# Kernel tuning notes

Hardware: AMD Instinct MI355X
Metric: run time of the kernel (lower is better)

The kernel has to match this reference:

```python
import jax, jax.numpy as jnp
import numpy as np
from jax import lax

T, N, H, A = 128, 64, 1024, 16  # timesteps, batch(envs), hidden_size, num_actions


def _ortho(key, shape):
    # approximate nn.init.orthogonal_ via QR of a gaussian
    a = jax.random.normal(key, shape, dtype=jnp.float32)
    flip = shape[0] < shape[1]
    q, r = jnp.linalg.qr(a.T if flip else a)
    q = q * jnp.sign(jnp.diagonal(r))
    return (q.T if flip else q).astype(jnp.float32)


def setup_inputs() -> dict:
    key = jax.random.key(0)
    ks = jax.random.split(key, 10)
    c = jax.random.normal(ks[0], (T * N, H), dtype=jnp.float32)
    hxs = jax.random.normal(ks[1], (N, 2 * H), dtype=jnp.float32)
    masks = jnp.ones((T * N, 1), dtype=jnp.float32)
    prev_action_one_hot = jax.random.uniform(ks[2], (T * N, A), dtype=jnp.float32)
    # GRUCell params (torch layout: weight_ih [3H, in], weight_hh [3H, H])
    w_ih_h = _ortho(ks[3], (3 * H, H))
    w_hh_h = _ortho(ks[4], (3 * H, H))
    b_ih_h = jnp.zeros((3 * H,), dtype=jnp.float32)
    b_hh_h = jnp.zeros((3 * H,), dtype=jnp.float32)
    w_ih_p = _ortho(ks[5], (3 * H, H))
    w_hh_p = _ortho(ks[6], (3 * H, H))
    b_ih_p = jnp.zeros((3 * H,), dtype=jnp.float32)
    b_hh_p = jnp.zeros((3 * H,), dtype=jnp.float32)
    # p_network: Linear(H+A, H) -> tanh -> Linear(H, A)
    p_w1 = jax.random.normal(ks[7], (H, H + A), dtype=jnp.float32) / np.sqrt(H + A)
    p_b1 = jnp.zeros((H,), dtype=jnp.float32)
    p_w2 = jax.random.normal(ks[8], (A, H), dtype=jnp.float32) / np.sqrt(H)
    p_b2 = jnp.zeros((A,), dtype=jnp.float32)
    return dict(c=c, hxs=hxs, masks=masks, prev_action_one_hot=prev_action_one_hot,
                w_ih_h=w_ih_h, w_hh_h=w_hh_h, b_ih_h=b_ih_h, b_hh_h=b_hh_h,
                w_ih_p=w_ih_p, w_hh_p=w_hh_p, b_ih_p=b_ih_p, b_hh_p=b_hh_p,
                p_w1=p_w1, p_b1=p_b1, p_w2=p_w2, p_b2=p_b2)


def _gru_cell(x, h, w_ih, w_hh, b_ih, b_hh):
    # torch.nn.GRUCell semantics
    gi = x @ w_ih.T + b_ih  # [N, 3H]
    gh = h @ w_hh.T + b_hh  # [N, 3H]
    i_r, i_z, i_n = jnp.split(gi, 3, axis=1)
    h_r, h_z, h_n = jnp.split(gh, 3, axis=1)
    r = jax.nn.sigmoid(i_r + h_r)
    z = jax.nn.sigmoid(i_z + h_z)
    n = jnp.tanh(i_n + r * h_n)
    return (1.0 - z) * n + z * h


def reference(c, hxs, masks, prev_action_one_hot,
              w_ih_h, w_hh_h, b_ih_h, b_hh_h,
              w_ih_p, w_hh_p, b_ih_p, b_hh_p,
              p_w1, p_b1, p_w2, p_b2):
    c3 = c.reshape(T, N, H)
    m3 = masks.reshape(T, N, 1)
    a3 = prev_action_one_hot.reshape(T, N, A)
    h0 = hxs[:, :H]
    pol0 = hxs[:, H:]

    def step(carry, xs):
        h, pol = carry
        c_t, m_t, a_t = xs
        p_in = jnp.concatenate([h, a_t], axis=1) * m_t
        p_dist = jnp.tanh(p_in @ p_w1.T + p_b1) @ p_w2.T + p_b2  # [N, A]
        h = _gru_cell(c_t, h * m_t, w_ih_h, w_hh_h, b_ih_h, b_hh_h)
        pol = _gru_cell(c_t, pol * m_t, w_ih_p, w_hh_p, b_ih_p, b_hh_p)
        return (h, pol), (p_dist, pol)

    (h, pol), (acc_p_dist, acc_policy) = lax.scan(step, (h0, pol0), (c3, m3, a3))
    acc_p_dist = acc_p_dist.reshape(T * N, -1)
    acc_policy = acc_policy.reshape(T * N, -1)
    hxs_out = jnp.concatenate([h, pol], axis=1)
    return acc_p_dist, acc_policy, hxs_out
```

## Files before the change

### kernel.cpp

```cpp
#include <hip/hip_runtime.h>
#include <hip/hip_bf16.h>
#include <math.h>

#define TT 128
#define NN 64
#define HH 1024
#define AA 16
#define G3 3072
#define NC 6144
#define PK 1088
#define WLDS_STRIDE 1032
#define GISL 3072

#define PD_OFF  0
#define POL_OFF (TT*NN*AA)
#define HXS_OFF (POL_OFF + TT*NN*HH)

typedef __attribute__((ext_vector_type(8))) short short8;
typedef __attribute__((ext_vector_type(4))) float f32x4;

__device__ __align__(16) __hip_bfloat16 g_c_bf[TT*NN*HH];
__device__ __align__(16) __hip_bfloat16 g_wihc_bf[NC*HH];
__device__ __align__(16) __hip_bfloat16 g_whh_bf[2][G3*HH];
__device__ __align__(16) __hip_bfloat16 g_pw1_bf[HH*PK];
__device__ __align__(16) __hip_bfloat16 g_pw2_bf[AA*HH];
__device__ float g_gi2[(size_t)2*64*TT*GISL];
__device__ float g_h[NN*HH];
__device__ float g_pol[NN*HH];
__device__ __align__(16) __hip_bfloat16 g_pin_all[(size_t)(TT+1)*NN*PK];
__device__ __align__(16) __hip_bfloat16 g_polm_all[(size_t)(TT+1)*NN*HH];
__device__ __align__(16) __hip_bfloat16 g_ph_all[TT*NN*HH];

__device__ __align__(256) unsigned g_flagsA[2][64];
__device__ __align__(256) unsigned g_gi_cnt[64];

__device__ __forceinline__ float sigmoidf_(float x) { return 1.0f / (1.0f + __expf(-x)); }
__device__ __forceinline__ float tanhf_(float x) {
  float e = __expf(2.0f * x);
  return 1.0f - 2.0f / (e + 1.0f);
}

__global__ __launch_bounds__(256) void conv_all(
    const float* __restrict__ c, const float* __restrict__ masks, const float* __restrict__ act,
    const float* __restrict__ wih_h, const float* __restrict__ wih_p,
    const float* __restrict__ whh_h, const float* __restrict__ whh_p,
    const float* __restrict__ pw1, const float* __restrict__ pw2)
{
  size_t i = (size_t)blockIdx.x * 256 + threadIdx.x;
  size_t stride = (size_t)gridDim.x * 256;
  for (size_t f = i; f < (size_t)TT*NN*HH; f += stride) g_c_bf[f] = __float2bfloat16(c[f]);
  for (size_t f = i; f < (size_t)G3*HH; f += stride) {
    g_wihc_bf[f]                 = __float2bfloat16(wih_h[f]);
    g_wihc_bf[(size_t)G3*HH + f] = __float2bfloat16(wih_p[f]);
    g_whh_bf[0][f] = __float2bfloat16(whh_h[f]);
    g_whh_bf[1][f] = __float2bfloat16(whh_p[f]);
  }
  for (size_t f = i; f < (size_t)HH*PK; f += stride) {
    int o = (int)(f / PK), j = (int)(f % PK);
    g_pw1_bf[f] = (j < HH + AA) ? __float2bfloat16(pw1[(size_t)o*(HH+AA) + j]) : __float2bfloat16(0.0f);
  }
  for (size_t f = i; f < (size_t)AA*HH; f += stride) g_pw2_bf[f] = __float2bfloat16(pw2[f]);
  for (size_t f = i; f < (size_t)TT*NN*(PK-HH); f += stride) {
    int row = (int)(f >> 6), j = (int)(f & 63);
    float v = (j < AA) ? act[(size_t)row*AA + j] * masks[row] : 0.0f;
    g_pin_all[(size_t)row*PK + HH + j] = __float2bfloat16(v);
  }
}

__global__ __launch_bounds__(256) void init_kernel(const float* __restrict__ hxs,
                                                   const float* __restrict__ masks) {
  int f = blockIdx.x * 256 + threadIdx.x;
  int n = f >> 10, j = f & 1023;
  float m0 = masks[n];
  float hv = hxs[n * 2 * HH + j];
  float pv = hxs[n * 2 * HH + HH + j];
  g_h[f] = hv;
  g_pol[f] = pv;
  g_pin_all[(size_t)n * PK + j]  = __float2bfloat16(hv * m0);
  g_polm_all[(size_t)n * HH + j] = __float2bfloat16(pv * m0);
  if (f < 128)
    __hip_atomic_store(&g_flagsA[f >> 6][f & 63], 0u,
                       __ATOMIC_RELAXED, __HIP_MEMORY_SCOPE_AGENT);
  if (f >= 128 && f < 192)
    __hip_atomic_store(&g_gi_cnt[f - 128], 0u,
                       __ATOMIC_RELAXED, __HIP_MEMORY_SCOPE_AGENT);
}

__global__ __launch_bounds__(256, 1) void fused_scan(
    const float* __restrict__ masks,
    const float* __restrict__ bih_h, const float* __restrict__ bhh_h,
    const float* __restrict__ bih_p, const float* __restrict__ bhh_p,
    float* __restrict__ out)
{
  extern __shared__ __align__(16) __hip_bfloat16 Dyn[];
  __shared__ float m_lds[TT * NN];
  __shared__ __align__(8) __hip_bfloat16 sL[NN * 16];
  const int tid = threadIdx.x, l = tid & 63, w = tid >> 6;

  if (blockIdx.x < 128) {
    __hip_bfloat16* Ws = Dyn;
    const int gru = blockIdx.x >> 6;
    const int idx = blockIdx.x & 63;
    const int c0  = idx * 16;
    const __hip_bfloat16* __restrict__ W = g_whh_bf[gru];

    for (int i = tid; i < TT * NN; i += 256) m_lds[i] = masks[i];

    for (int ch = tid; ch < 48 * 128; ch += 256) {
      int row = ch >> 7, ko = (ch & 127) * 8;
      int gate = row >> 4, j = row & 15;
      *(short8*)(&Ws[row * WLDS_STRIDE + ko]) =
          *(const short8*)(W + (size_t)(gate * HH + c0 + j) * HH + ko);
    }
    __syncthreads();

    const float* bi = (gru == 0) ? bih_h : bih_p;
    const float* bh = (gru == 0) ? bhh_h : bhh_p;
    const int col = c0 + (l & 15);
    const float bir = bi[col],        bhr = bh[col];
    const float biz = bi[HH + col],   bhz = bh[HH + col];
    const float bin = bi[2*HH + col], bhn = bh[2*HH + col];
    const int rowbase = w * 16 + (l >> 4) * 4;
    const int arow = w * 16 + (l & 15);
    const int lo8 = (l >> 4) * 8;
    const int jj = l & 15;

    float hst[4];
    {
      const float* st0 = (gru == 0) ? g_h : g_pol;
#pragma unroll
      for (int reg = 0; reg < 4; ++reg) hst[reg] = st0[(rowbase + reg) * HH + col];
    }

    while (__hip_atomic_load(&g_gi_cnt[0], __ATOMIC_RELAXED,
                             __HIP_MEMORY_SCOPE_AGENT) < 48u) { }
    const float* __restrict__ gib = g_gi2 + (size_t)(gru * 64 + idx) * TT * GISL;
    float gir[4], giz[4], gin[4];
#pragma unroll
    for (int reg = 0; reg < 4; ++reg) {
      const float* gp = gib + (size_t)(rowbase + reg) * 48;
      gir[reg] = gp[jj]; giz[reg] = gp[16 + jj]; gin[reg] = gp[32 + jj];
    }

    const int astr = (gru == 0) ? PK : HH;
    volatile unsigned* __restrict__ myflags = g_flagsA[gru];

    for (int t = 0; t < TT; ++t) {
      const __hip_bfloat16* __restrict__ Ab =
          (gru == 0) ? (g_pin_all + (size_t)t * NN * PK)
                     : (g_polm_all + (size_t)t * NN * HH);
      const __hip_bfloat16* __restrict__ arowp = Ab + (size_t)arow * astr + lo8;

      short8 av[32];
#pragma unroll
      for (int u = 0; u < 32; ++u) av[u] = *(const short8*)(arowp + u * 32);

      f32x4 acc0 = {}, acc1 = {}, acc2 = {};
#pragma unroll
      for (int u = 0; u < 32; ++u) {
        short8 b0  = *(const short8*)(&Ws[( 0 + jj) * WLDS_STRIDE + u * 32 + lo8]);
        short8 b1  = *(const short8*)(&Ws[(16 + jj) * WLDS_STRIDE + u * 32 + lo8]);
        short8 bn2 = *(const short8*)(&Ws[(32 + jj) * WLDS_STRIDE + u * 32 + lo8]);
        acc0 = __builtin_amdgcn_mfma_f32_16x16x32_bf16(av[u], b0,  acc0, 0, 0, 0);
        acc1 = __builtin_amdgcn_mfma_f32_16x16x32_bf16(av[u], b1,  acc1, 0, 0, 0);
        acc2 = __builtin_amdgcn_mfma_f32_16x16x32_bf16(av[u], bn2, acc2, 0, 0, 0);
      }

      float hv_out[4];
#pragma unroll
      for (int reg = 0; reg < 4; ++reg) {
        int row = rowbase + reg;
        float mk  = m_lds[t * NN + row];
        float mk1 = (t < TT - 1) ? m_lds[(t + 1) * NN + row] : 1.0f;
        float hm = hst[reg] * mk;
        float rg  = sigmoidf_(gir[reg] + acc0[reg] + bir + bhr);
        float z   = sigmoidf_(giz[reg] + acc1[reg] + biz + bhz);
        float nn2 = tanhf_  (gin[reg] + bin + rg * (acc2[reg] + bhn));
        float hv = (1.0f - z) * nn2 + z * hm;
        hst[reg] = hv;
        hv_out[reg] = hv;
        sL[row * 16 + jj] = __float2bfloat16(hv * mk1);
      }

      __syncthreads();
      {
        int rr = tid >> 2, cc = tid & 3;
        unsigned long long v = *(const unsigned long long*)(&sL[rr * 16 + cc * 4]);
        __hip_bfloat16* dstp = (gru == 0)
            ? (g_pin_all + (size_t)(t + 1) * NN * PK + (size_t)rr * PK + c0 + cc * 4)
            : (g_polm_all + (size_t)(t + 1) * NN * HH + (size_t)rr * HH + c0 + cc * 4);
        __hip_atomic_store((unsigned long long*)dstp, v,
                           __ATOMIC_RELAXED, __HIP_MEMORY_SCOPE_AGENT);
      }

      if (t < TT - 1) {
        asm volatile("s_waitcnt vmcnt(0)" ::: "memory");
        __syncthreads();
        if (tid == 0)
          __hip_atomic_store((unsigned*)&g_flagsA[gru][idx], (unsigned)(t + 1),
                             __ATOMIC_RELAXED, __HIP_MEMORY_SCOPE_AGENT);
        if (gru == 1) {
#pragma unroll
          for (int reg = 0; reg < 4; ++reg)
            out[POL_OFF + (size_t)(t * NN + rowbase + reg) * HH + col] = hv_out[reg];
        }
        {
          const int slab = (t + 1) >> 1;
          while (__hip_atomic_load(&g_gi_cnt[slab], __ATOMIC_RELAXED,
                                   __HIP_MEMORY_SCOPE_AGENT) < 48u) { }
          const float* gpt = gib + (size_t)(t + 1) * GISL;
#pragma unroll
          for (int reg = 0; reg < 4; ++reg) {
            const float* gp = gpt + (size_t)(rowbase + reg) * 48;
            gir[reg] = gp[jj]; giz[reg] = gp[16 + jj]; gin[reg] = gp[32 + jj];
          }
        }
        while (__hip_atomic_load((const unsigned*)&myflags[l], __ATOMIC_RELAXED,
                                 __HIP_MEMORY_SCOPE_AGENT) < (unsigned)(t + 1)) { }
      } else {
        if (gru == 1) {
#pragma unroll
          for (int reg = 0; reg < 4; ++reg)
            out[POL_OFF + (size_t)(t * NN + rowbase + reg) * HH + col] = hv_out[reg];
        }
      }
    }

    float* stf = (gru == 0) ? g_h : g_pol;
#pragma unroll
    for (int reg = 0; reg < 4; ++reg) stf[(rowbase + reg) * HH + col] = hst[reg];

  } else {
    __hip_bfloat16* AsD = Dyn;
    __hip_bfloat16* BsD = Dyn + 2 * 128 * 72;
    const int roff = (w >> 1) * 64, coff = (w & 1) * 64;

    for (int kt2 = 0; kt2 < 24; ++kt2) {
      const int tile = (blockIdx.x - 128) + (kt2 << 7);
      const int bm = tile / 48, bn = tile % 48;
      const __hip_bfloat16* A = g_c_bf    + (size_t)bm * 128 * HH;
      const __hip_bfloat16* B = g_wihc_bf + (size_t)bn * 128 * HH;

      short8 ra[4], rb[4];
#define PG_LOAD(KT) { _Pragma("unroll") for (int q = 0; q < 4; ++q) { \
    int cch = q * 256 + tid; int row = cch >> 3, ko = (cch & 7) * 8; \
    ra[q] = *(const short8*)(A + (size_t)row * HH + (KT) * 64 + ko); \
    rb[q] = *(const short8*)(B + (size_t)row * HH + (KT) * 64 + ko); } }
#define PG_STORE(BUF) { _Pragma("unroll") for (int q = 0; q < 4; ++q) { \
    int cch = q * 256 + tid; int row = cch >> 3, ko = (cch & 7) * 8; \
    *(short8*)(AsD + (BUF) * 9216 + row * 72 + ko) = ra[q]; \
    *(short8*)(BsD + (BUF) * 9216 + row * 72 + ko) = rb[q]; } }

      __syncthreads();
      PG_LOAD(0); PG_STORE(0);
      f32x4 acc[4][4] = {};
      for (int kt = 0; kt < 16; ++kt) {
        __syncthreads();
        if (kt < 15) PG_LOAD(kt + 1);
        const int buf = kt & 1;
#pragma unroll
        for (int ks = 0; ks < 2; ++ks) {
          short8 a[4], b[4];
#pragma unroll
          for (int fr = 0; fr < 4; ++fr)
            a[fr] = *(const short8*)(AsD + buf * 9216 + (roff + fr * 16 + (l & 15)) * 72 + ks * 32 + (l >> 4) * 8);
#pragma unroll
          for (int fc = 0; fc < 4; ++fc)
            b[fc] = *(const short8*)(BsD + buf * 9216 + (coff + fc * 16 + (l & 15)) * 72 + ks * 32 + (l >> 4) * 8);
#pragma unroll
          for (int fr = 0; fr < 4; ++fr)
#pragma unroll
            for (int fc = 0; fc < 4; ++fc)
              acc[fr][fc] = __builtin_amdgcn_mfma_f32_16x16x32_bf16(a[fr], b[fc], acc[fr][fc], 0, 0, 0);
        }
        if (kt < 15) PG_STORE((kt + 1) & 1);
      }
#pragma unroll
      for (int fr = 0; fr < 4; ++fr)
#pragma unroll
        for (int fc = 0; fc < 4; ++fc) {
          int colg = bn * 128 + coff + fc * 16 + (l & 15);
          int q2 = colg >> 10;
          int gru2 = (q2 >= 3), gate = q2 - 3 * gru2;
          int hcol = colg & 1023, cb = hcol >> 4, j = hcol & 15;
#pragma unroll
          for (int reg = 0; reg < 4; ++reg) {
            int grow = bm * 128 + roff + fr * 16 + (l >> 4) * 4 + reg;
            int tt2 = grow >> 6, n = grow & 63;
            __hip_atomic_store(
                &g_gi2[((size_t)(gru2 * 64 + cb) * TT + tt2) * GISL + n * 48 + gate * 16 + j],
                acc[fr][fc][reg], __ATOMIC_RELAXED, __HIP_MEMORY_SCOPE_AGENT);
          }
        }
      asm volatile("s_waitcnt vmcnt(0)" ::: "memory");
      __syncthreads();
      if (tid == 0)
        __hip_atomic_fetch_add(&g_gi_cnt[bm], 1u,
                               __ATOMIC_RELAXED, __HIP_MEMORY_SCOPE_AGENT);
    }
  }
}

__global__ __launch_bounds__(256) void pol_gemm(const float* __restrict__ pb1) {
  __shared__ __align__(16) __hip_bfloat16 As[2][128 * 72];
  __shared__ __align__(16) __hip_bfloat16 Bs[2][128 * 72];
  const int tid = threadIdx.x, l = tid & 63, w = tid >> 6;
  const int bm = blockIdx.x / 8, bn = blockIdx.x % 8;
  const __hip_bfloat16* A = g_pin_all + (size_t)bm * 128 * PK;
  const __hip_bfloat16* B = g_pw1_bf  + (size_t)bn * 128 * PK;
  const int roff = (w >> 1) * 64, coff = (w & 1) * 64;

  short8 ra[4], rb[4];
#define PL_LOAD(KT) { _Pragma("unroll") for (int q = 0; q < 4; ++q) { \
    int cch = q * 256 + tid; int row = cch >> 3, ko = (cch & 7) * 8; \
    ra[q] = *(const short8*)(A + (size_t)row * PK + (KT) * 64 + ko); \
    rb[q] = *(const short8*)(B + (size_t)row * PK + (KT) * 64 + ko); } }
#define PL_STORE(BUF) { _Pragma("unroll") for (int q = 0; q < 4; ++q) { \
    int cch = q * 256 + tid; int row = cch >> 3, ko = (cch & 7) * 8; \
    *(short8*)(&As[BUF][row * 72 + ko]) = ra[q]; \
    *(short8*)(&Bs[BUF][row * 72 + ko]) = rb[q]; } }

  PL_LOAD(0); PL_STORE(0);
  f32x4 acc[4][4] = {};
  for (int kt = 0; kt < 17; ++kt) {
    __syncthreads();
    if (kt < 16) PL_LOAD(kt + 1);
    const int buf = kt & 1;
#pragma unroll
    for (int ks = 0; ks < 2; ++ks) {
      short8 a[4], b[4];
#pragma unroll
      for (int fr = 0; fr < 4; ++fr)
        a[fr] = *(const short8*)(&As[buf][(roff + fr * 16 + (l & 15)) * 72 + ks * 32 + (l >> 4) * 8]);
#pragma unroll
      for (int fc = 0; fc < 4; ++fc)
        b[fc] = *(const short8*)(&Bs[buf][(coff + fc * 16 + (l & 15)) * 72 + ks * 32 + (l >> 4) * 8]);
#pragma unroll
      for (int fr = 0; fr < 4; ++fr)
#pragma unroll
        for (int fc = 0; fc < 4; ++fc)
          acc[fr][fc] = __builtin_amdgcn_mfma_f32_16x16x32_bf16(a[fr], b[fc], acc[fr][fc], 0, 0, 0);
    }
    if (kt < 16) PL_STORE((kt + 1) & 1);
  }
#pragma unroll
  for (int fc = 0; fc < 4; ++fc) {
    int col = bn * 128 + coff + fc * 16 + (l & 15);
    float b1v = pb1[col];
#pragma unroll
    for (int fr = 0; fr < 4; ++fr)
#pragma unroll
      for (int reg = 0; reg < 4; ++reg) {
        int row = bm * 128 + roff + fr * 16 + (l >> 4) * 4 + reg;
        g_ph_all[(size_t)row * HH + col] = __float2bfloat16(tanhf_(acc[fr][fc][reg] + b1v));
      }
  }
}

__global__ __launch_bounds__(256) void pdist_kernel(const float* __restrict__ pb2,
                                                    float* __restrict__ out) {
  const int tid = threadIdx.x, l = tid & 63, w = tid >> 6;
  const int r0 = blockIdx.x * 64;
  f32x4 pa = {};
  const __hip_bfloat16* PH = g_ph_all + (size_t)(r0 + w * 16 + (l & 15)) * HH;
  const __hip_bfloat16* B  = g_pw2_bf + (size_t)(l & 15) * HH;
#pragma unroll 4
  for (int k32 = 0; k32 < 32; ++k32) {
    short8 a = *(const short8*)(PH + k32 * 32 + (l >> 4) * 8);
    short8 b = *(const short8*)(B  + k32 * 32 + (l >> 4) * 8);
    pa = __builtin_amdgcn_mfma_f32_16x16x32_bf16(a, b, pa, 0, 0, 0);
  }
  int o = l & 15;
  float bb = pb2[o];
#pragma unroll
  for (int reg = 0; reg < 4; ++reg) {
    int row = r0 + w * 16 + (l >> 4) * 4 + reg;
    out[PD_OFF + (size_t)row * AA + o] = pa[reg] + bb;
  }
}

__global__ __launch_bounds__(256) void final_kernel(float* __restrict__ out) {
  int f = blockIdx.x * 256 + threadIdx.x;
  int n = f >> 11, j = f & 2047;
  out[HXS_OFF + f] = (j < HH) ? g_h[n * HH + j] : g_pol[n * HH + (j - HH)];
}

extern "C" void kernel_launch(void* const* d_in, const int* in_sizes, int n_in,
                              void* d_out, int out_size, void* d_ws, size_t ws_size,
                              hipStream_t stream) {
  const float* c     = (const float*)d_in[0];
  const float* hxs   = (const float*)d_in[1];
  const float* masks = (const float*)d_in[2];
  const float* act   = (const float*)d_in[3];
  const float* wih_h = (const float*)d_in[4];
  const float* whh_h = (const float*)d_in[5];
  const float* bih_h = (const float*)d_in[6];
  const float* bhh_h = (const float*)d_in[7];
  const float* wih_p = (const float*)d_in[8];
  const float* whh_p = (const float*)d_in[9];
  const float* bih_p = (const float*)d_in[10];
  const float* bhh_p = (const float*)d_in[11];
  const float* pw1   = (const float*)d_in[12];
  const float* pb1   = (const float*)d_in[13];
  const float* pw2   = (const float*)d_in[14];
  const float* pb2   = (const float*)d_in[15];
  float* out = (float*)d_out;

  const int dyn_bytes = 48 * WLDS_STRIDE * 2;
  (void)hipFuncSetAttribute((const void*)fused_scan,
                            hipFuncAttributeMaxDynamicSharedMemorySize, dyn_bytes);

  conv_all<<<4096, 256, 0, stream>>>(c, masks, act, wih_h, wih_p, whh_h, whh_p, pw1, pw2);
  init_kernel<<<256, 256, 0, stream>>>(hxs, masks);
  fused_scan<<<256, 256, dyn_bytes, stream>>>(masks, bih_h, bhh_h, bih_p, bhh_p, out);
  pol_gemm<<<512, 256, 0, stream>>>(pb1);
  pdist_kernel<<<128, 256, 0, stream>>>(pb2, out);
  final_kernel<<<512, 256, 0, stream>>>(out);
}
```

Measured before the change: 1.223 ms.

## Fuse policy GEMM and pdist into scan kernel's idle helper blocks

```diff
diff --git a/kernel.cpp b/kernel.cpp
--- a/kernel.cpp
+++ b/kernel.cpp
@@ -21,7 +21,6 @@
 
 __device__ __align__(16) __hip_bfloat16 g_c_bf[TT*NN*HH];
 __device__ __align__(16) __hip_bfloat16 g_wihc_bf[NC*HH];
-__device__ __align__(16) __hip_bfloat16 g_whh_bf[2][G3*HH];
 __device__ __align__(16) __hip_bfloat16 g_pw1_bf[HH*PK];
 __device__ __align__(16) __hip_bfloat16 g_pw2_bf[AA*HH];
 __device__ float g_gi2[(size_t)2*64*TT*GISL];
@@ -33,6 +32,7 @@
 
 __device__ __align__(256) unsigned g_flagsA[2][64];
 __device__ __align__(256) unsigned g_gi_cnt[64];
+__device__ __align__(256) unsigned g_pol_cnt[64];
 
 __device__ __forceinline__ float sigmoidf_(float x) { return 1.0f / (1.0f + __expf(-x)); }
 __device__ __forceinline__ float tanhf_(float x) {
@@ -43,7 +43,6 @@
 __global__ __launch_bounds__(256) void conv_all(
     const float* __restrict__ c, const float* __restrict__ masks, const float* __restrict__ act,
     const float* __restrict__ wih_h, const float* __restrict__ wih_p,
-    const float* __restrict__ whh_h, const float* __restrict__ whh_p,
     const float* __restrict__ pw1, const float* __restrict__ pw2)
 {
   size_t i = (size_t)blockIdx.x * 256 + threadIdx.x;
@@ -52,8 +51,6 @@
   for (size_t f = i; f < (size_t)G3*HH; f += stride) {
     g_wihc_bf[f]                 = __float2bfloat16(wih_h[f]);
     g_wihc_bf[(size_t)G3*HH + f] = __float2bfloat16(wih_p[f]);
-    g_whh_bf[0][f] = __float2bfloat16(whh_h[f]);
-    g_whh_bf[1][f] = __float2bfloat16(whh_p[f]);
   }
   for (size_t f = i; f < (size_t)HH*PK; f += stride) {
     int o = (int)(f / PK), j = (int)(f % PK);
@@ -84,12 +81,17 @@
   if (f >= 128 && f < 192)
     __hip_atomic_store(&g_gi_cnt[f - 128], 0u,
                        __ATOMIC_RELAXED, __HIP_MEMORY_SCOPE_AGENT);
+  if (f >= 192 && f < 256)
+    __hip_atomic_store(&g_pol_cnt[f - 192], 0u,
+                       __ATOMIC_RELAXED, __HIP_MEMORY_SCOPE_AGENT);
 }
 
 __global__ __launch_bounds__(256, 1) void fused_scan(
     const float* __restrict__ masks,
+    const float* __restrict__ whh_h, const float* __restrict__ whh_p,
     const float* __restrict__ bih_h, const float* __restrict__ bhh_h,
     const float* __restrict__ bih_p, const float* __restrict__ bhh_p,
+    const float* __restrict__ pb1, const float* __restrict__ pb2,
     float* __restrict__ out)
 {
   extern __shared__ __align__(16) __hip_bfloat16 Dyn[];
@@ -102,15 +104,18 @@
     const int gru = blockIdx.x >> 6;
     const int idx = blockIdx.x & 63;
     const int c0  = idx * 16;
-    const __hip_bfloat16* __restrict__ W = g_whh_bf[gru];
+    const float* __restrict__ Wf = (gru == 0) ? whh_h : whh_p;
 
     for (int i = tid; i < TT * NN; i += 256) m_lds[i] = masks[i];
 
     for (int ch = tid; ch < 48 * 128; ch += 256) {
       int row = ch >> 7, ko = (ch & 127) * 8;
       int gate = row >> 4, j = row & 15;
-      *(short8*)(&Ws[row * WLDS_STRIDE + ko]) =
-          *(const short8*)(W + (size_t)(gate * HH + c0 + j) * HH + ko);
+      const float* s = Wf + (size_t)(gate * HH + c0 + j) * HH + ko;
+      union { short8 v; __hip_bfloat16 hh[8]; } tmp;
+#pragma unroll
+      for (int q = 0; q < 8; ++q) tmp.hh[q] = __float2bfloat16(s[q]);
+      *(short8*)(&Ws[row * WLDS_STRIDE + ko]) = tmp.v;
     }
     __syncthreads();
 
@@ -132,8 +137,11 @@
       for (int reg = 0; reg < 4; ++reg) hst[reg] = st0[(rowbase + reg) * HH + col];
     }
 
+    unsigned gi_ready = 0;
     while (__hip_atomic_load(&g_gi_cnt[0], __ATOMIC_RELAXED,
                              __HIP_MEMORY_SCOPE_AGENT) < 48u) { }
+    asm volatile("" ::: "memory");
+    gi_ready = 1;
     const float* __restrict__ gib = g_gi2 + (size_t)(gru * 64 + idx) * TT * GISL;
     float gir[4], giz[4], gin[4];
 #pragma unroll
@@ -143,7 +151,6 @@
     }
 
     const int astr = (gru == 0) ? PK : HH;
-    volatile unsigned* __restrict__ myflags = g_flagsA[gru];
 
     for (int t = 0; t < TT; ++t) {
       const __hip_bfloat16* __restrict__ Ab =
@@ -151,9 +158,22 @@
                      : (g_polm_all + (size_t)t * NN * HH);
       const __hip_bfloat16* __restrict__ arowp = Ab + (size_t)arow * astr + lo8;
 
+      unsigned fv = __hip_atomic_load(&g_flagsA[gru][l], __ATOMIC_RELAXED,
+                                      __HIP_MEMORY_SCOPE_AGENT);
+      unsigned long long rdy = __ballot(fv >= (unsigned)t);
       short8 av[32];
 #pragma unroll
-      for (int u = 0; u < 32; ++u) av[u] = *(const short8*)(arowp + u * 32);
+      for (int g = 0; g < 8; ++g) {
+        while (((rdy >> (g * 8)) & 0xFFull) != 0xFFull) {
+          fv = __hip_atomic_load(&g_flagsA[gru][l], __ATOMIC_RELAXED,
+                                 __HIP_MEMORY_SCOPE_AGENT);
+          rdy = __ballot(fv >= (unsigned)t);
+        }
+        asm volatile("" ::: "memory");
+#pragma unroll
+        for (int q = 0; q < 4; ++q)
+          av[g * 4 + q] = *(const short8*)(arowp + (g * 4 + q) * 32);
+      }
 
       f32x4 acc0 = {}, acc1 = {}, acc2 = {};
 #pragma unroll
@@ -192,10 +212,10 @@
         __hip_atomic_store((unsigned long long*)dstp, v,
                            __ATOMIC_RELAXED, __HIP_MEMORY_SCOPE_AGENT);
       }
+      asm volatile("s_waitcnt vmcnt(0)" ::: "memory");
+      __syncthreads();
 
       if (t < TT - 1) {
-        asm volatile("s_waitcnt vmcnt(0)" ::: "memory");
-        __syncthreads();
         if (tid == 0)
           __hip_atomic_store((unsigned*)&g_flagsA[gru][idx], (unsigned)(t + 1),
                              __ATOMIC_RELAXED, __HIP_MEMORY_SCOPE_AGENT);
@@ -205,9 +225,13 @@
             out[POL_OFF + (size_t)(t * NN + rowbase + reg) * HH + col] = hv_out[reg];
         }
         {
-          const int slab = (t + 1) >> 1;
-          while (__hip_atomic_load(&g_gi_cnt[slab], __ATOMIC_RELAXED,
-                                   __HIP_MEMORY_SCOPE_AGENT) < 48u) { }
+          const unsigned slab = (unsigned)((t + 1) >> 1);
+          if (slab >= gi_ready) {
+            while (__hip_atomic_load(&g_gi_cnt[slab], __ATOMIC_RELAXED,
+                                     __HIP_MEMORY_SCOPE_AGENT) < 48u) { }
+            asm volatile("" ::: "memory");
+            gi_ready = slab + 1;
+          }
           const float* gpt = gib + (size_t)(t + 1) * GISL;
 #pragma unroll
           for (int reg = 0; reg < 4; ++reg) {
@@ -215,8 +239,6 @@
             gir[reg] = gp[jj]; giz[reg] = gp[16 + jj]; gin[reg] = gp[32 + jj];
           }
         }
-        while (__hip_atomic_load((const unsigned*)&myflags[l], __ATOMIC_RELAXED,
-                                 __HIP_MEMORY_SCOPE_AGENT) < (unsigned)(t + 1)) { }
       } else {
         if (gru == 1) {
 #pragma unroll
@@ -234,46 +256,41 @@
     __hip_bfloat16* AsD = Dyn;
     __hip_bfloat16* BsD = Dyn + 2 * 128 * 72;
     const int roff = (w >> 1) * 64, coff = (w & 1) * 64;
+    const int pid = blockIdx.x - 128;
 
     for (int kt2 = 0; kt2 < 24; ++kt2) {
-      const int tile = (blockIdx.x - 128) + (kt2 << 7);
+      const int tile = pid + (kt2 << 7);
       const int bm = tile / 48, bn = tile % 48;
       const __hip_bfloat16* A = g_c_bf    + (size_t)bm * 128 * HH;
       const __hip_bfloat16* B = g_wihc_bf + (size_t)bn * 128 * HH;
 
       short8 ra[4], rb[4];
-#define PG_LOAD(KT) { _Pragma("unroll") for (int q = 0; q < 4; ++q) { \
+#define PG_LOAD(KT, AP, BP, STR) { _Pragma("unroll") for (int q = 0; q < 4; ++q) { \
     int cch = q * 256 + tid; int row = cch >> 3, ko = (cch & 7) * 8; \
-    ra[q] = *(const short8*)(A + (size_t)row * HH + (KT) * 64 + ko); \
-    rb[q] = *(const short8*)(B + (size_t)row * HH + (KT) * 64 + ko); } }
+    ra[q] = *(const short8*)((AP) + (size_t)row * (STR) + (KT) * 64 + ko); \
+    rb[q] = *(const short8*)((BP) + (size_t)row * (STR) + (KT) * 64 + ko); } }
 #define PG_STORE(BUF) { _Pragma("unroll") for (int q = 0; q < 4; ++q) { \
     int cch = q * 256 + tid; int row = cch >> 3, ko = (cch & 7) * 8; \
     *(short8*)(AsD + (BUF) * 9216 + row * 72 + ko) = ra[q]; \
     *(short8*)(BsD + (BUF) * 9216 + row * 72 + ko) = rb[q]; } }
-
-      __syncthreads();
-      PG_LOAD(0); PG_STORE(0);
+#define PG_MMA(BUF) { _Pragma("unroll") for (int ks = 0; ks < 2; ++ks) { \
+      short8 a[4], b[4]; \
+      _Pragma("unroll") for (int fr = 0; fr < 4; ++fr) \
+        a[fr] = *(const short8*)(AsD + (BUF) * 9216 + (roff + fr * 16 + (l & 15)) * 72 + ks * 32 + (l >> 4) * 8); \
+      _Pragma("unroll") for (int fc = 0; fc < 4; ++fc) \
+        b[fc] = *(const short8*)(BsD + (BUF) * 9216 + (coff + fc * 16 + (l & 15)) * 72 + ks * 32 + (l >> 4) * 8); \
+      _Pragma("unroll") for (int fr = 0; fr < 4; ++fr) \
+        _Pragma("unroll") for (int fc = 0; fc < 4; ++fc) \
+          acc[fr][fc] = __builtin_amdgcn_mfma_f32_16x16x32_bf16(a[fr], b[fc], acc[fr][fc], 0, 0, 0); } }
+
+      __syncthreads();
+      PG_LOAD(0, A, B, HH) PG_STORE(0)
       f32x4 acc[4][4] = {};
       for (int kt = 0; kt < 16; ++kt) {
         __syncthreads();
-        if (kt < 15) PG_LOAD(kt + 1);
-        const int buf = kt & 1;
-#pragma unroll
-        for (int ks = 0; ks < 2; ++ks) {
-          short8 a[4], b[4];
-#pragma unroll
-          for (int fr = 0; fr < 4; ++fr)
-            a[fr] = *(const short8*)(AsD + buf * 9216 + (roff + fr * 16 + (l & 15)) * 72 + ks * 32 + (l >> 4) * 8);
-#pragma unroll
-          for (int fc = 0; fc < 4; ++fc)
-            b[fc] = *(const short8*)(BsD + buf * 9216 + (coff + fc * 16 + (l & 15)) * 72 + ks * 32 + (l >> 4) * 8);
-#pragma unroll
-          for (int fr = 0; fr < 4; ++fr)
-#pragma unroll
-            for (int fc = 0; fc < 4; ++fc)
-              acc[fr][fc] = __builtin_amdgcn_mfma_f32_16x16x32_bf16(a[fr], b[fc], acc[fr][fc], 0, 0, 0);
-        }
-        if (kt < 15) PG_STORE((kt + 1) & 1);
+        if (kt < 15) PG_LOAD(kt + 1, A, B, HH)
+        PG_MMA(kt & 1)
+        if (kt < 15) PG_STORE((kt + 1) & 1)
       }
 #pragma unroll
       for (int fr = 0; fr < 4; ++fr)
@@ -298,84 +315,77 @@
         __hip_atomic_fetch_add(&g_gi_cnt[bm], 1u,
                                __ATOMIC_RELAXED, __HIP_MEMORY_SCOPE_AGENT);
     }
-  }
-}
-
-__global__ __launch_bounds__(256) void pol_gemm(const float* __restrict__ pb1) {
-  __shared__ __align__(16) __hip_bfloat16 As[2][128 * 72];
-  __shared__ __align__(16) __hip_bfloat16 Bs[2][128 * 72];
-  const int tid = threadIdx.x, l = tid & 63, w = tid >> 6;
-  const int bm = blockIdx.x / 8, bn = blockIdx.x % 8;
-  const __hip_bfloat16* A = g_pin_all + (size_t)bm * 128 * PK;
-  const __hip_bfloat16* B = g_pw1_bf  + (size_t)bn * 128 * PK;
-  const int roff = (w >> 1) * 64, coff = (w & 1) * 64;
-
-  short8 ra[4], rb[4];
-#define PL_LOAD(KT) { _Pragma("unroll") for (int q = 0; q < 4; ++q) { \
-    int cch = q * 256 + tid; int row = cch >> 3, ko = (cch & 7) * 8; \
-    ra[q] = *(const short8*)(A + (size_t)row * PK + (KT) * 64 + ko); \
-    rb[q] = *(const short8*)(B + (size_t)row * PK + (KT) * 64 + ko); } }
-#define PL_STORE(BUF) { _Pragma("unroll") for (int q = 0; q < 4; ++q) { \
-    int cch = q * 256 + tid; int row = cch >> 3, ko = (cch & 7) * 8; \
-    *(short8*)(&As[BUF][row * 72 + ko]) = ra[q]; \
-    *(short8*)(&Bs[BUF][row * 72 + ko]) = rb[q]; } }
-
-  PL_LOAD(0); PL_STORE(0);
-  f32x4 acc[4][4] = {};
-  for (int kt = 0; kt < 17; ++kt) {
-    __syncthreads();
-    if (kt < 16) PL_LOAD(kt + 1);
-    const int buf = kt & 1;
-#pragma unroll
-    for (int ks = 0; ks < 2; ++ks) {
-      short8 a[4], b[4];
-#pragma unroll
-      for (int fr = 0; fr < 4; ++fr)
-        a[fr] = *(const short8*)(&As[buf][(roff + fr * 16 + (l & 15)) * 72 + ks * 32 + (l >> 4) * 8]);
-#pragma unroll
-      for (int fc = 0; fc < 4; ++fc)
-        b[fc] = *(const short8*)(&Bs[buf][(coff + fc * 16 + (l & 15)) * 72 + ks * 32 + (l >> 4) * 8]);
-#pragma unroll
-      for (int fr = 0; fr < 4; ++fr)
-#pragma unroll
-        for (int fc = 0; fc < 4; ++fc)
-          acc[fr][fc] = __builtin_amdgcn_mfma_f32_16x16x32_bf16(a[fr], b[fc], acc[fr][fc], 0, 0, 0);
-    }
-    if (kt < 16) PL_STORE((kt + 1) & 1);
-  }
-#pragma unroll
-  for (int fc = 0; fc < 4; ++fc) {
-    int col = bn * 128 + coff + fc * 16 + (l & 15);
-    float b1v = pb1[col];
-#pragma unroll
-    for (int fr = 0; fr < 4; ++fr)
+
+    for (int k2 = 0; k2 < 4; ++k2) {
+      const int tile = (k2 << 7) + pid;
+      const int bm = tile >> 3, bn = tile & 7;
+      const unsigned need = (unsigned)(2 * bm + 1);
+      {
+        unsigned fv;
+        do {
+          fv = __hip_atomic_load(&g_flagsA[0][l], __ATOMIC_RELAXED,
+                                 __HIP_MEMORY_SCOPE_AGENT);
+        } while (!__all(fv >= need));
+        asm volatile("" ::: "memory");
+      }
+      const __hip_bfloat16* A = g_pin_all + (size_t)bm * 128 * PK;
+      const __hip_bfloat16* B = g_pw1_bf  + (size_t)bn * 128 * PK;
+
+      short8 ra[4], rb[4];
+      __syncthreads();
+      PG_LOAD(0, A, B, PK) PG_STORE(0)
+      f32x4 acc[4][4] = {};
+      for (int kt = 0; kt < 17; ++kt) {
+        __syncthreads();
+        if (kt < 16) PG_LOAD(kt + 1, A, B, PK)
+        PG_MMA(kt & 1)
+        if (kt < 16) PG_STORE((kt + 1) & 1)
+      }
+#pragma unroll
+      for (int fc = 0; fc < 4; ++fc) {
+        int colg = bn * 128 + coff + fc * 16 + (l & 15);
+        float b1v = pb1[colg];
+#pragma unroll
+        for (int fr = 0; fr < 4; ++fr)
+#pragma unroll
+          for (int reg = 0; reg < 4; ++reg) {
+            int row = bm * 128 + roff + fr * 16 + (l >> 4) * 4 + reg;
+            __hip_bfloat16 hb = __float2bfloat16(tanhf_(acc[fr][fc][reg] + b1v));
+            __hip_atomic_store((unsigned short*)&g_ph_all[(size_t)row * HH + colg],
+                               *(unsigned short*)&hb,
+                               __ATOMIC_RELAXED, __HIP_MEMORY_SCOPE_AGENT);
+          }
+      }
+      asm volatile("s_waitcnt vmcnt(0)" ::: "memory");
+      __syncthreads();
+      if (tid == 0)
+        __hip_atomic_fetch_add(&g_pol_cnt[bm], 1u,
+                               __ATOMIC_RELAXED, __HIP_MEMORY_SCOPE_AGENT);
+    }
+
+    {
+      const int r0 = pid * 64;
+      const int bm2 = pid >> 1;
+      while (__hip_atomic_load(&g_pol_cnt[bm2], __ATOMIC_RELAXED,
+                               __HIP_MEMORY_SCOPE_AGENT) < 8u) { }
+      asm volatile("" ::: "memory");
+      f32x4 pa = {};
+      const __hip_bfloat16* PH = g_ph_all + (size_t)(r0 + w * 16 + (l & 15)) * HH;
+      const __hip_bfloat16* B  = g_pw2_bf + (size_t)(l & 15) * HH;
+#pragma unroll 4
+      for (int k32 = 0; k32 < 32; ++k32) {
+        short8 a = *(const short8*)(PH + k32 * 32 + (l >> 4) * 8);
+        short8 b = *(const short8*)(B  + k32 * 32 + (l >> 4) * 8);
+        pa = __builtin_amdgcn_mfma_f32_16x16x32_bf16(a, b, pa, 0, 0, 0);
+      }
+      int o = l & 15;
+      float bb = pb2[o];
 #pragma unroll
       for (int reg = 0; reg < 4; ++reg) {
-        int row = bm * 128 + roff + fr * 16 + (l >> 4) * 4 + reg;
-        g_ph_all[(size_t)row * HH + col] = __float2bfloat16(tanhf_(acc[fr][fc][reg] + b1v));
-      }
-  }
-}
-
-__global__ __launch_bounds__(256) void pdist_kernel(const float* __restrict__ pb2,
-                                                    float* __restrict__ out) {
-  const int tid = threadIdx.x, l = tid & 63, w = tid >> 6;
-  const int r0 = blockIdx.x * 64;
-  f32x4 pa = {};
-  const __hip_bfloat16* PH = g_ph_all + (size_t)(r0 + w * 16 + (l & 15)) * HH;
-  const __hip_bfloat16* B  = g_pw2_bf + (size_t)(l & 15) * HH;
-#pragma unroll 4
-  for (int k32 = 0; k32 < 32; ++k32) {
-    short8 a = *(const short8*)(PH + k32 * 32 + (l >> 4) * 8);
-    short8 b = *(const short8*)(B  + k32 * 32 + (l >> 4) * 8);
-    pa = __builtin_amdgcn_mfma_f32_16x16x32_bf16(a, b, pa, 0, 0, 0);
-  }
-  int o = l & 15;
-  float bb = pb2[o];
-#pragma unroll
-  for (int reg = 0; reg < 4; ++reg) {
-    int row = r0 + w * 16 + (l >> 4) * 4 + reg;
-    out[PD_OFF + (size_t)row * AA + o] = pa[reg] + bb;
+        int row = r0 + w * 16 + (l >> 4) * 4 + reg;
+        out[PD_OFF + (size_t)row * AA + o] = pa[reg] + bb;
+      }
+    }
   }
 }
 
@@ -410,10 +420,10 @@
   (void)hipFuncSetAttribute((const void*)fused_scan,
                             hipFuncAttributeMaxDynamicSharedMemorySize, dyn_bytes);
 
-  conv_all<<<4096, 256, 0, stream>>>(c, masks, act, wih_h, wih_p, whh_h, whh_p, pw1, pw2);
+  conv_all<<<4096, 256, 0, stream>>>(c, masks, act, wih_h, wih_p, pw1, pw2);
   init_kernel<<<256, 256, 0, stream>>>(hxs, masks);
-  fused_scan<<<256, 256, dyn_bytes, stream>>>(masks, bih_h, bhh_h, bih_p, bhh_p, out);
-  pol_gemm<<<512, 256, 0, stream>>>(pb1);
-  pdist_kernel<<<128, 256, 0, stream>>>(pb2, out);
+  fused_scan<<<256, 256, dyn_bytes, stream>>>(masks, whh_h, whh_p,
+                                              bih_h, bhh_h, bih_p, bhh_p,
+                                              pb1, pb2, out);
   final_kernel<<<512, 256, 0, stream>>>(out);
 }
```

Result: faster. 1.067 ms, median of 2 (-12.8%).
